# Kernel tuning notes

Hardware: AMD Instinct MI355X
Metric: run time of the kernel (lower is better)

## Reference

```python
import jax, jax.numpy as jnp
import numpy as np

N_NODES = 50000
N_EDGES = 800000
N_GRAPHS = 64
D_IN = 128
DIMS = (256, 256)


def _glorot(key, shape):
    fan_in, fan_out = shape[0], shape[1]
    lim = jnp.sqrt(6.0 / (fan_in + fan_out)).astype(jnp.float32)
    return jax.random.uniform(key, shape, jnp.float32, -lim, lim)


def setup_inputs() -> dict:
    key = jax.random.key(0)
    ks = jax.random.split(key, 12)
    x = jax.random.normal(ks[0], (N_NODES, D_IN), dtype=jnp.float32)
    edge_index = jax.random.randint(ks[1], (2, N_EDGES), 0, N_NODES, dtype=jnp.int64)
    batch = jnp.sort(jax.random.randint(ks[2], (N_NODES,), 0, N_GRAPHS, dtype=jnp.int64))
    # MLP params per GIN layer: Linear(in,dim) -> ReLU -> Linear(dim,dim) -> ReLU
    W1_0 = _glorot(ks[3], (D_IN, DIMS[0]))
    b1_0 = jnp.zeros((DIMS[0],), jnp.float32)
    W2_0 = _glorot(ks[4], (DIMS[0], DIMS[0]))
    b2_0 = jnp.zeros((DIMS[0],), jnp.float32)
    W1_1 = _glorot(ks[5], (DIMS[0], DIMS[1]))
    b1_1 = jnp.zeros((DIMS[1],), jnp.float32)
    W2_1 = _glorot(ks[6], (DIMS[1], DIMS[1]))
    b2_1 = jnp.zeros((DIMS[1],), jnp.float32)
    return {"x": x, "edge_index": edge_index, "batch": batch,
            "W1_0": W1_0, "b1_0": b1_0, "W2_0": W2_0, "b2_0": b2_0,
            "W1_1": W1_1, "b1_1": b1_1, "W2_1": W2_1, "b2_1": b2_1}


def _gin_layer(x, src, dst, W1, b1, W2, b2):
    # aggregate: sum of neighbor features (messages from src into dst)
    agg = jax.ops.segment_sum(x[src], dst, num_segments=N_NODES)
    h = x + agg  # (1 + eps) * x + agg, eps = 0
    h = jax.nn.relu(h @ W1 + b1)
    h = jax.nn.relu(h @ W2 + b2)
    return h


def reference(x, edge_index, batch, W1_0, b1_0, W2_0, b2_0, W1_1, b1_1, W2_1, b2_1):
    src, dst = edge_index[0], edge_index[1]
    h = _gin_layer(x, src, dst, W1_0, b1_0, W2_0, b2_0)
    h = _gin_layer(h, src, dst, W1_1, b1_1, W2_1, b2_1)
    # global mean pool over graphs
    sums = jax.ops.segment_sum(h, batch, num_segments=N_GRAPHS)
    counts = jax.ops.segment_sum(jnp.ones((h.shape[0],), h.dtype), batch, num_segments=N_GRAPHS)
    return sums / jnp.maximum(counts, 1.0)[:, None]
```

## Files before the change

kernel.cpp:

```cpp
#include <hip/hip_runtime.h>


typedef __bf16 bf16x8 __attribute__((ext_vector_type(8)));
typedef float f32x4 __attribute__((ext_vector_type(4)));

#define N_NODES 50000
#define N_EDGES 800000
#define N_GRAPHS 64
#define SCAN_BLOCKS 196

#define PB_HIST0 3125
#define PB_P0    6250
#define PB_P1    6378
#define PB_P2    6634
#define PB_P3    6890
#define PB_BIAS  7146
#define PB_TOTAL 7150

#define OFF_FLAGS  0ull
#define OFF_WB     64ull
#define OFF_WP0    4096ull
#define OFF_WP1    (OFF_WP0 + 65536ull)
#define OFF_WP2    (OFF_WP1 + 131072ull)
#define OFF_WP3    (OFF_WP2 + 131072ull)
#define OFF_CNT    462848ull
#define OFF_ROWPTR 662864ull
#define OFF_CURSOR 862880ull
#define OFF_SSRC   1062912ull
#define OFF_A      2662912ull
#define OFF_B      15462912ull
#define OFF_C      41062912ull
#define OFF_POOL32 66662912ull
#define OFF_BSUM   66728448ull
#define OFF_DCNT   66730496ull
#define OFF_DCUR   66731520ull
#define OFF_PERM   66732544ull

__device__ __forceinline__ float b2f(unsigned short u) {
  union { unsigned int i; float f; } v; v.i = ((unsigned int)u) << 16; return v.f;
}
__device__ __forceinline__ float b2f_lo(unsigned int u) {
  union { unsigned int i; float f; } v; v.i = u << 16; return v.f;
}
__device__ __forceinline__ float b2f_hi(unsigned int u) {
  union { unsigned int i; float f; } v; v.i = u & 0xffff0000u; return v.f;
}
__device__ __forceinline__ unsigned short f2b(float f) {
  union { unsigned int i; float f; } v; v.f = f;
  unsigned int r = v.i + 0x7fffu + ((v.i >> 16) & 1u);
  return (unsigned short)(r >> 16);
}

__global__ void detect_zero(const unsigned int* __restrict__ xw,
                            const unsigned int* __restrict__ eiw,
                            int* __restrict__ flags,
                            int* __restrict__ counts, float* __restrict__ pool32,
                            int* __restrict__ dcnt) {
  if (blockIdx.x == 0) {
    __shared__ int s_f[256], s_i[256];
    int t = threadIdx.x;
    int fh = 0, iz = 0;
    for (int i = t; i < 1024; i += 256) {
      unsigned int e = (xw[i] >> 7) & 0xFFu;
      fh += (e >= 115u && e <= 130u) ? 1 : 0;
      iz += (eiw[2 * i + 1] == 0u) ? 1 : 0;
    }
    s_f[t] = fh; s_i[t] = iz;
    __syncthreads();
    for (int s = 128; s > 0; s >>= 1) {
      if (t < s) { s_f[t] += s_f[t + s]; s_i[t] += s_i[t + s]; }
      __syncthreads();
    }
    if (t == 0) { flags[0] = s_f[0] > 512 ? 1 : 0; flags[1] = s_i[0] > 512 ? 1 : 0; }
  } else {
    int i = (blockIdx.x - 1) * 256 + threadIdx.x;
    if (i < N_NODES) counts[i] = 0;
    if (i < N_GRAPHS * 256) pool32[i] = 0.f;
    if (i < 256) dcnt[i] = 0;
  }
}

__device__ __forceinline__ void pack_w_elem(const void* W, unsigned short* Wp,
                                            int e, int isb) {
  int n = e & 255;
  int krow = e >> 8;
  int kb = krow >> 5, r = krow & 31;
  int q = r >> 3, j = r & 7;
  size_t out = ((((size_t)(kb << 8) + n) << 2) + q) * 8 + j;
  Wp[out] = isb ? ((const unsigned short*)W)[e] : f2b(((const float*)W)[e]);
}

__global__ void prep_kernel(const void* __restrict__ x, const int* __restrict__ ei,
                            const void* W0, const void* W1, const void* W2, const void* W3,
                            const void* b0, const void* b1, const void* b2, const void* b3,
                            unsigned short* __restrict__ A,
                            int* __restrict__ counts,
                            unsigned short* __restrict__ Wp0, unsigned short* __restrict__ Wp1,
                            unsigned short* __restrict__ Wp2, unsigned short* __restrict__ Wp3,
                            unsigned short* __restrict__ Wb,
                            const int* __restrict__ flags) {
  int b = blockIdx.x, t = threadIdx.x;
  int isb = flags[0];
  if (b < PB_HIST0) {
    if (!isb) {
      int i = b * 256 + t;
      const float4* f = (const float4*)x;
      float4 a = f[2 * i], c = f[2 * i + 1];
      ushort4 o0; o0.x = f2b(a.x); o0.y = f2b(a.y); o0.z = f2b(a.z); o0.w = f2b(a.w);
      ushort4 o1; o1.x = f2b(c.x); o1.y = f2b(c.y); o1.z = f2b(c.z); o1.w = f2b(c.w);
      ((ushort4*)A)[2 * i] = o0;
      ((ushort4*)A)[2 * i + 1] = o1;
    }
  } else if (b < PB_P0) {
    int e = (b - PB_HIST0) * 256 + t;
    int dst = flags[1] ? ei[2 * (N_EDGES + e)] : ei[N_EDGES + e];
    atomicAdd(&counts[dst], 1);
  } else if (b < PB_P1) {
    pack_w_elem(W0, Wp0, (b - PB_P0) * 256 + t, isb);
  } else if (b < PB_P2) {
    pack_w_elem(W1, Wp1, (b - PB_P1) * 256 + t, isb);
  } else if (b < PB_P3) {
    pack_w_elem(W2, Wp2, (b - PB_P2) * 256 + t, isb);
  } else if (b < PB_BIAS) {
    pack_w_elem(W3, Wp3, (b - PB_P3) * 256 + t, isb);
  } else {
    int i = (b - PB_BIAS) * 256 + t;
    const void* p = (i < 256) ? b0 : (i < 512) ? b1 : (i < 768) ? b2 : b3;
    int n = i & 255;
    Wb[i] = isb ? ((const unsigned short*)p)[n] : f2b(((const float*)p)[n]);
  }
}

__global__ void scan_blocks(const int* __restrict__ counts,
                            int* __restrict__ rowptr, int* __restrict__ bsum,
                            int* __restrict__ dcnt) {
  __shared__ int sd[256], lh[256];
  int t = threadIdx.x;
  int i = blockIdx.x * 256 + t;
  int v = (i < N_NODES) ? counts[i] : 0;
  sd[t] = v;
  lh[t] = 0;
  __syncthreads();
  if (i < N_NODES) atomicAdd(&lh[v > 255 ? 255 : v], 1);
  __syncthreads();
  if (lh[t] > 0) atomicAdd(&dcnt[t], lh[t]);
  for (int off = 1; off < 256; off <<= 1) {
    int u = (t >= off) ? sd[t - off] : 0;
    __syncthreads();
    sd[t] += u;
    __syncthreads();
  }
  if (i < N_NODES) rowptr[i] = sd[t] - v;
  if (t == 255) bsum[blockIdx.x] = sd[255];
}

__global__ void deg_scan(const int* __restrict__ dcnt, int* __restrict__ dcur) {
  __shared__ int sd[256];
  int t = threadIdx.x;
  int v = dcnt[t];
  sd[t] = v;
  __syncthreads();
  for (int off = 1; off < 256; off <<= 1) {
    int u = (t >= off) ? sd[t - off] : 0;
    __syncthreads();
    sd[t] += u;
    __syncthreads();
  }
  dcur[t] = sd[t] - v;
}

__global__ void scan_fix(int* __restrict__ rowptr, int* __restrict__ cursor,
                         const int* __restrict__ bsum, const int* __restrict__ counts,
                         int* __restrict__ dcur, int* __restrict__ perm) {
  __shared__ int sb[256], base[256], lc[256];
  int t = threadIdx.x;
  sb[t] = (t < SCAN_BLOCKS) ? bsum[t] : 0;
  lc[t] = 0;
  __syncthreads();
  for (int off = 1; off < 256; off <<= 1) {
    int u = (t >= off) ? sb[t - off] : 0;
    __syncthreads();
    sb[t] += u;
    __syncthreads();
  }
  int boffv = (blockIdx.x > 0) ? sb[blockIdx.x - 1] : 0;
  int i = blockIdx.x * 256 + t;
  int d = 0;
  if (i < N_NODES) {
    int v = rowptr[i] + boffv;
    rowptr[i] = v;
    cursor[i] = v;
    int c = counts[i];
    d = c > 255 ? 255 : c;
    atomicAdd(&lc[d], 1);
  }
  if (i == 0) rowptr[N_NODES] = N_EDGES;
  __syncthreads();
  int cnt = lc[t];
  base[t] = (cnt > 0) ? atomicAdd(&dcur[t], cnt) : 0;
  __syncthreads();
  lc[t] = 0;
  __syncthreads();
  if (i < N_NODES) {
    int r = atomicAdd(&lc[d], 1);
    perm[base[d] + r] = i;
  }
}

__global__ void fill_kernel(const int* __restrict__ ei, int* __restrict__ cursor,
                            unsigned short* __restrict__ ssrc,
                            const int* __restrict__ flags) {
  int e = blockIdx.x * blockDim.x + threadIdx.x;
  if (e >= N_EDGES) return;
  int is64 = flags[1];
  int src = is64 ? ei[2 * e] : ei[e];
  int dst = is64 ? ei[2 * (N_EDGES + e)] : ei[N_EDGES + e];
  int pos = atomicAdd(&cursor[dst], 1);
  ssrc[pos] = (unsigned short)src;
}

__global__ void fused_gather_gemm(const unsigned short* __restrict__ featCanon,
                                  const unsigned short* __restrict__ featRaw,
                                  const int* __restrict__ rowptr,
                                  const unsigned short* __restrict__ ssrc,
                                  const int* __restrict__ perm,
                                  const unsigned short* __restrict__ Wp,
                                  const unsigned short* __restrict__ Wb, int bias_row,
                                  unsigned short* __restrict__ C, int D,
                                  const int* __restrict__ flags) {
  __shared__ __align__(16) unsigned short Alds[16 * 264];
  __shared__ int sp[16];
  const int S = D + 8;
  const int row0 = blockIdx.x << 4;
  const int lane = threadIdx.x & 63;
  const int wave = threadIdx.x >> 6;
  const unsigned short* feat = flags[0] ? featRaw : featCanon;
  if (threadIdx.x < 16) sp[threadIdx.x] = perm[row0 + threadIdx.x];
  __syncthreads();

  {
    int sub = lane >> 4;
    int l = lane & 15;
    int nl = (wave << 2) + sub;
    int node = sp[nl];
    int beg = rowptr[node], end = rowptr[node + 1];
    int c = l << 3;
    if (D == 256) {
      const unsigned short* spt = feat + (size_t)node * 256 + c;
      uint4 sv0 = *(const uint4*)spt;
      uint4 sv1 = *(const uint4*)(spt + 128);
      float a0 = b2f_lo(sv0.x), a1 = b2f_hi(sv0.x), a2 = b2f_lo(sv0.y), a3 = b2f_hi(sv0.y);
      float a4 = b2f_lo(sv0.z), a5 = b2f_hi(sv0.z), a6 = b2f_lo(sv0.w), a7 = b2f_hi(sv0.w);
      float a8 = b2f_lo(sv1.x), a9 = b2f_hi(sv1.x), aA = b2f_lo(sv1.y), aB = b2f_hi(sv1.y);
      float aC = b2f_lo(sv1.z), aD = b2f_hi(sv1.z), aE = b2f_lo(sv1.w), aF = b2f_hi(sv1.w);
      int i = beg;
      for (; i + 1 < end; i += 2) {
        int s0 = ssrc[i], s1 = ssrc[i + 1];
        const unsigned short* p0 = feat + (size_t)s0 * 256 + c;
        const unsigned short* p1 = feat + (size_t)s1 * 256 + c;
        uint4 v00 = *(const uint4*)p0;
        uint4 v01 = *(const uint4*)(p0 + 128);
        uint4 v10 = *(const uint4*)p1;
        uint4 v11 = *(const uint4*)(p1 + 128);
        a0 += b2f_lo(v00.x); a1 += b2f_hi(v00.x); a2 += b2f_lo(v00.y); a3 += b2f_hi(v00.y);
        a4 += b2f_lo(v00.z); a5 += b2f_hi(v00.z); a6 += b2f_lo(v00.w); a7 += b2f_hi(v00.w);
        a8 += b2f_lo(v01.x); a9 += b2f_hi(v01.x); aA += b2f_lo(v01.y); aB += b2f_hi(v01.y);
        aC += b2f_lo(v01.z); aD += b2f_hi(v01.z); aE += b2f_lo(v01.w); aF += b2f_hi(v01.w);
        a0 += b2f_lo(v10.x); a1 += b2f_hi(v10.x); a2 += b2f_lo(v10.y); a3 += b2f_hi(v10.y);
        a4 += b2f_lo(v10.z); a5 += b2f_hi(v10.z); a6 += b2f_lo(v10.w); a7 += b2f_hi(v10.w);
        a8 += b2f_lo(v11.x); a9 += b2f_hi(v11.x); aA += b2f_lo(v11.y); aB += b2f_hi(v11.y);
        aC += b2f_lo(v11.z); aD += b2f_hi(v11.z); aE += b2f_lo(v11.w); aF += b2f_hi(v11.w);
      }
      if (i < end) {
        const unsigned short* p0 = feat + (size_t)ssrc[i] * 256 + c;
        uint4 v00 = *(const uint4*)p0;
        uint4 v01 = *(const uint4*)(p0 + 128);
        a0 += b2f_lo(v00.x); a1 += b2f_hi(v00.x); a2 += b2f_lo(v00.y); a3 += b2f_hi(v00.y);
        a4 += b2f_lo(v00.z); a5 += b2f_hi(v00.z); a6 += b2f_lo(v00.w); a7 += b2f_hi(v00.w);
        a8 += b2f_lo(v01.x); a9 += b2f_hi(v01.x); aA += b2f_lo(v01.y); aB += b2f_hi(v01.y);
        aC += b2f_lo(v01.z); aD += b2f_hi(v01.z); aE += b2f_lo(v01.w); aF += b2f_hi(v01.w);
      }
      uint4 o0, o1;
      o0.x = ((unsigned int)f2b(a1) << 16) | f2b(a0);
      o0.y = ((unsigned int)f2b(a3) << 16) | f2b(a2);
      o0.z = ((unsigned int)f2b(a5) << 16) | f2b(a4);
      o0.w = ((unsigned int)f2b(a7) << 16) | f2b(a6);
      o1.x = ((unsigned int)f2b(a9) << 16) | f2b(a8);
      o1.y = ((unsigned int)f2b(aB) << 16) | f2b(aA);
      o1.z = ((unsigned int)f2b(aD) << 16) | f2b(aC);
      o1.w = ((unsigned int)f2b(aF) << 16) | f2b(aE);
      *(uint4*)(&Alds[nl * S + c]) = o0;
      *(uint4*)(&Alds[nl * S + c + 128]) = o1;
    } else {
      const unsigned short* spt = feat + (size_t)node * 128 + c;
      uint4 sv0 = *(const uint4*)spt;
      float a0 = b2f_lo(sv0.x), a1 = b2f_hi(sv0.x), a2 = b2f_lo(sv0.y), a3 = b2f_hi(sv0.y);
      float a4 = b2f_lo(sv0.z), a5 = b2f_hi(sv0.z), a6 = b2f_lo(sv0.w), a7 = b2f_hi(sv0.w);
      int i = beg;
      for (; i + 1 < end; i += 2) {
        int s0 = ssrc[i], s1 = ssrc[i + 1];
        uint4 v0 = *(const uint4*)(feat + (size_t)s0 * 128 + c);
        uint4 v1 = *(const uint4*)(feat + (size_t)s1 * 128 + c);
        a0 += b2f_lo(v0.x); a1 += b2f_hi(v0.x); a2 += b2f_lo(v0.y); a3 += b2f_hi(v0.y);
        a4 += b2f_lo(v0.z); a5 += b2f_hi(v0.z); a6 += b2f_lo(v0.w); a7 += b2f_hi(v0.w);
        a0 += b2f_lo(v1.x); a1 += b2f_hi(v1.x); a2 += b2f_lo(v1.y); a3 += b2f_hi(v1.y);
        a4 += b2f_lo(v1.z); a5 += b2f_hi(v1.z); a6 += b2f_lo(v1.w); a7 += b2f_hi(v1.w);
      }
      if (i < end) {
        uint4 v0 = *(const uint4*)(feat + (size_t)ssrc[i] * 128 + c);
        a0 += b2f_lo(v0.x); a1 += b2f_hi(v0.x); a2 += b2f_lo(v0.y); a3 += b2f_hi(v0.y);
        a4 += b2f_lo(v0.z); a5 += b2f_hi(v0.z); a6 += b2f_lo(v0.w); a7 += b2f_hi(v0.w);
      }
      uint4 o0;
      o0.x = ((unsigned int)f2b(a1) << 16) | f2b(a0);
      o0.y = ((unsigned int)f2b(a3) << 16) | f2b(a2);
      o0.z = ((unsigned int)f2b(a5) << 16) | f2b(a4);
      o0.w = ((unsigned int)f2b(a7) << 16) | f2b(a6);
      *(uint4*)(&Alds[nl * S + c]) = o0;
    }
  }
  __syncthreads();

  const int m = lane & 15;
  const int q = lane >> 4;
  f32x4 acc[4];
#pragma unroll
  for (int t = 0; t < 4; ++t) acc[t] = (f32x4){0.f, 0.f, 0.f, 0.f};

  const unsigned short* arow = &Alds[m * S + (q << 3)];
  const int nb = (wave << 6) + m;
  const int kblocks = D >> 5;
  for (int kb = 0; kb < kblocks; ++kb) {
    bf16x8 af = *(const bf16x8*)(arow + (kb << 5));
    const unsigned short* wp = Wp + (((size_t)(kb << 8) + nb) * 4 + q) * 8;
    bf16x8 b0 = *(const bf16x8*)(wp);
    bf16x8 b1 = *(const bf16x8*)(wp + 512);
    bf16x8 b2 = *(const bf16x8*)(wp + 1024);
    bf16x8 b3 = *(const bf16x8*)(wp + 1536);
    acc[0] = __builtin_amdgcn_mfma_f32_16x16x32_bf16(af, b0, acc[0], 0, 0, 0);
    acc[1] = __builtin_amdgcn_mfma_f32_16x16x32_bf16(af, b1, acc[1], 0, 0, 0);
    acc[2] = __builtin_amdgcn_mfma_f32_16x16x32_bf16(af, b2, acc[2], 0, 0, 0);
    acc[3] = __builtin_amdgcn_mfma_f32_16x16x32_bf16(af, b3, acc[3], 0, 0, 0);
  }
#pragma unroll
  for (int t = 0; t < 4; ++t) {
    int n = (wave << 6) + (t << 4) + m;
    float bv = b2f(Wb[bias_row * 256 + n]);
#pragma unroll
    for (int i = 0; i < 4; ++i) {
      int r = sp[(q << 2) + i];
      float v = fmaxf(acc[t][i] + bv, 0.f);
      C[(size_t)r * 256 + n] = f2b(v);
    }
  }
}

__global__ void gemm_relu(const unsigned short* __restrict__ A,
                          const unsigned short* __restrict__ Wp,
                          const unsigned short* __restrict__ Wb, int bias_row,
                          unsigned short* __restrict__ C, int K) {
  const int row0 = blockIdx.x << 4;
  const int lane = threadIdx.x & 63;
  const int wave = threadIdx.x >> 6;
  const int m = lane & 15;
  const int q = lane >> 4;
  f32x4 acc[4];
#pragma unroll
  for (int t = 0; t < 4; ++t) acc[t] = (f32x4){0.f, 0.f, 0.f, 0.f};

  const unsigned short* arow = A + (size_t)(row0 + m) * K + (q << 3);
  const int nb = (wave << 6) + m;
  const int kblocks = K >> 5;
  for (int kb = 0; kb < kblocks; ++kb) {
    bf16x8 af = *(const bf16x8*)(arow + (kb << 5));
    const unsigned short* wp = Wp + (((size_t)(kb << 8) + nb) * 4 + q) * 8;
    bf16x8 b0 = *(const bf16x8*)(wp);
    bf16x8 b1 = *(const bf16x8*)(wp + 512);
    bf16x8 b2 = *(const bf16x8*)(wp + 1024);
    bf16x8 b3 = *(const bf16x8*)(wp + 1536);
    acc[0] = __builtin_amdgcn_mfma_f32_16x16x32_bf16(af, b0, acc[0], 0, 0, 0);
    acc[1] = __builtin_amdgcn_mfma_f32_16x16x32_bf16(af, b1, acc[1], 0, 0, 0);
    acc[2] = __builtin_amdgcn_mfma_f32_16x16x32_bf16(af, b2, acc[2], 0, 0, 0);
    acc[3] = __builtin_amdgcn_mfma_f32_16x16x32_bf16(af, b3, acc[3], 0, 0, 0);
  }
#pragma unroll
  for (int t = 0; t < 4; ++t) {
    int n = (wave << 6) + (t << 4) + m;
    float bv = b2f(Wb[bias_row * 256 + n]);
#pragma unroll
    for (int i = 0; i < 4; ++i) {
      int r = row0 + (q << 2) + i;
      float v = fmaxf(acc[t][i] + bv, 0.f);
      C[(size_t)r * 256 + n] = f2b(v);
    }
  }
}

__global__ void gemm_pool(const unsigned short* __restrict__ A,
                          const unsigned short* __restrict__ Wp,
                          const unsigned short* __restrict__ Wb, int bias_row,
                          float* __restrict__ pool32, const int* __restrict__ batch,
                          const int* __restrict__ flags, int K) {
  __shared__ int sg[16];
  const int row0 = blockIdx.x << 4;
  const int lane = threadIdx.x & 63;
  const int wave = threadIdx.x >> 6;
  if (threadIdx.x < 16) {
    int r = row0 + threadIdx.x;
    sg[threadIdx.x] = flags[1] ? batch[2 * r] : batch[r];
  }
  __syncthreads();

  const int m = lane & 15;
  const int q = lane >> 4;
  f32x4 acc[4];
#pragma unroll
  for (int t = 0; t < 4; ++t) acc[t] = (f32x4){0.f, 0.f, 0.f, 0.f};

  const unsigned short* arow = A + (size_t)(row0 + m) * K + (q << 3);
  const int nb = (wave << 6) + m;
  const int kblocks = K >> 5;
  for (int kb = 0; kb < kblocks; ++kb) {
    bf16x8 af = *(const bf16x8*)(arow + (kb << 5));
    const unsigned short* wp = Wp + (((size_t)(kb << 8) + nb) * 4 + q) * 8;
    bf16x8 b0 = *(const bf16x8*)(wp);
    bf16x8 b1 = *(const bf16x8*)(wp + 512);
    bf16x8 b2 = *(const bf16x8*)(wp + 1024);
    bf16x8 b3 = *(const bf16x8*)(wp + 1536);
    acc[0] = __builtin_amdgcn_mfma_f32_16x16x32_bf16(af, b0, acc[0], 0, 0, 0);
    acc[1] = __builtin_amdgcn_mfma_f32_16x16x32_bf16(af, b1, acc[1], 0, 0, 0);
    acc[2] = __builtin_amdgcn_mfma_f32_16x16x32_bf16(af, b2, acc[2], 0, 0, 0);
    acc[3] = __builtin_amdgcn_mfma_f32_16x16x32_bf16(af, b3, acc[3], 0, 0, 0);
  }

  int uniform = (sg[0] == sg[15]);
#pragma unroll
  for (int t = 0; t < 4; ++t) {
    int n = (wave << 6) + (t << 4) + m;
    float bv = b2f(Wb[bias_row * 256 + n]);
    float v0 = fmaxf(acc[t][0] + bv, 0.f);
    float v1 = fmaxf(acc[t][1] + bv, 0.f);
    float v2 = fmaxf(acc[t][2] + bv, 0.f);
    float v3 = fmaxf(acc[t][3] + bv, 0.f);
    if (uniform) {
      float ps = v0 + v1 + v2 + v3;
      ps += __shfl_xor(ps, 16);
      ps += __shfl_xor(ps, 32);
      if (q == 0) unsafeAtomicAdd(&pool32[sg[0] * 256 + n], ps);
    } else {
      int gp = sg[q << 2];
      float a = 0.f;
      float vv[4] = {v0, v1, v2, v3};
#pragma unroll
      for (int i = 0; i < 4; ++i) {
        int g = sg[(q << 2) + i];
        if (g != gp) { unsafeAtomicAdd(&pool32[gp * 256 + n], a); a = 0.f; gp = g; }
        a += vv[i];
      }
      unsafeAtomicAdd(&pool32[gp * 256 + n], a);
    }
  }
}

__device__ __forceinline__ int lower_bound(const int* a, int n, int v, int is64) {
  int lo = 0, hi = n;
  while (lo < hi) {
    int mid = (lo + hi) >> 1;
    int bv = is64 ? a[2 * mid] : a[mid];
    if (bv < v) lo = mid + 1; else hi = mid;
  }
  return lo;
}

__global__ void pool_final(const float* __restrict__ pool32,
                           const int* __restrict__ batch,
                           void* __restrict__ out,
                           const int* __restrict__ flags) {
  __shared__ int sh[2];
  int g = blockIdx.x;
  int is64 = flags[1];
  if (threadIdx.x == 0) sh[0] = lower_bound(batch, N_NODES, g, is64);
  if (threadIdx.x == 1) sh[1] = lower_bound(batch, N_NODES, g + 1, is64);
  __syncthreads();
  int c = threadIdx.x;
  float res = pool32[g * 256 + c] / fmaxf((float)(sh[1] - sh[0]), 1.0f);
  if (flags[0]) ((unsigned short*)out)[(size_t)g * 256 + c] = f2b(res);
  else          ((float*)out)[(size_t)g * 256 + c] = res;
}

extern "C" void kernel_launch(void* const* d_in, const int* in_sizes, int n_in,
                              void* d_out, int out_size, void* d_ws, size_t ws_size,
                              hipStream_t stream) {
  const void* x    = d_in[0];
  const int*  ei   = (const int*)d_in[1];
  const int*  batch= (const int*)d_in[2];

  char* ws = (char*)d_ws;
  int*            flags = (int*)(ws + OFF_FLAGS);
  unsigned short* Wb    = (unsigned short*)(ws + OFF_WB);
  unsigned short* Wp0   = (unsigned short*)(ws + OFF_WP0);
  unsigned short* Wp1   = (unsigned short*)(ws + OFF_WP1);
  unsigned short* Wp2   = (unsigned short*)(ws + OFF_WP2);
  unsigned short* Wp3   = (unsigned short*)(ws + OFF_WP3);
  int*            cnts  = (int*)(ws + OFF_CNT);
  int*            rowp  = (int*)(ws + OFF_ROWPTR);
  int*            curs  = (int*)(ws + OFF_CURSOR);
  unsigned short* ssrc  = (unsigned short*)(ws + OFF_SSRC);
  unsigned short* A     = (unsigned short*)(ws + OFF_A);
  unsigned short* B     = (unsigned short*)(ws + OFF_B);
  unsigned short* C     = (unsigned short*)(ws + OFF_C);
  float*          pool32= (float*)(ws + OFF_POOL32);
  int*            bsum  = (int*)(ws + OFF_BSUM);
  int*            dcnt  = (int*)(ws + OFF_DCNT);
  int*            dcur  = (int*)(ws + OFF_DCUR);
  int*            perm  = (int*)(ws + OFF_PERM);

  detect_zero<<<197, 256, 0, stream>>>((const unsigned int*)x, (const unsigned int*)ei,
                                       flags, cnts, pool32, dcnt);
  prep_kernel<<<PB_TOTAL, 256, 0, stream>>>(x, ei,
                                            d_in[3], d_in[5], d_in[7], d_in[9],
                                            d_in[4], d_in[6], d_in[8], d_in[10],
                                            A, cnts, Wp0, Wp1, Wp2, Wp3, Wb, flags);
  scan_blocks<<<SCAN_BLOCKS, 256, 0, stream>>>(cnts, rowp, bsum, dcnt);
  deg_scan<<<1, 256, 0, stream>>>(dcnt, dcur);
  scan_fix<<<SCAN_BLOCKS, 256, 0, stream>>>(rowp, curs, bsum, cnts, dcur, perm);
  fill_kernel<<<3125, 256, 0, stream>>>(ei, curs, ssrc, flags);

  fused_gather_gemm<<<3125, 256, 0, stream>>>(A, (const unsigned short*)x, rowp, ssrc,
                                              perm, Wp0, Wb, 0, C, 128, flags);
  gemm_relu<<<3125, 256, 0, stream>>>(C, Wp1, Wb, 1, B, 256);

  fused_gather_gemm<<<3125, 256, 0, stream>>>(B, B, rowp, ssrc,
                                              perm, Wp2, Wb, 2, C, 256, flags);
  gemm_pool<<<3125, 256, 0, stream>>>(C, Wp3, Wb, 3, pool32, batch, flags, 256);

  pool_final<<<N_GRAPHS, 256, 0, stream>>>(pool32, batch, d_out, flags);
}
```

Before: 383.7 us.

## Replicate pool accumulators, fold degree scan into scan_fix, unroll gather by four

Pooling atomics now target one of eight replicated per-graph accumulator buffers chosen by block index, and pool_final sums the replicas. This is meant to cut atomic contention on the 64x256 pool array. The single-block deg_scan kernel is removed: every scan_fix block recomputes the degree-histogram prefix locally, and dcur is now zeroed as a counter. The gather loop is unrolled to four edges per iteration so more loads are in flight, at the cost of more registers.

After: 378.2 us. About the same (-1.4%).

```diff
diff --git a/kernel.cpp b/kernel.cpp
--- a/kernel.cpp
+++ b/kernel.cpp
@@ -8,6 +8,7 @@
 #define N_EDGES 800000
 #define N_GRAPHS 64
 #define SCAN_BLOCKS 196
+#define NREP 8
 
 #define PB_HIST0 3125
 #define PB_P0    6250
@@ -31,10 +32,10 @@
 #define OFF_B      15462912ull
 #define OFF_C      41062912ull
 #define OFF_POOL32 66662912ull
-#define OFF_BSUM   66728448ull
-#define OFF_DCNT   66730496ull
-#define OFF_DCUR   66731520ull
-#define OFF_PERM   66732544ull
+#define OFF_BSUM   67187200ull
+#define OFF_DCNT   67189248ull
+#define OFF_DCUR   67190272ull
+#define OFF_PERM   67191296ull
 
 __device__ __forceinline__ float b2f(unsigned short u) {
   union { unsigned int i; float f; } v; v.i = ((unsigned int)u) << 16; return v.f;
@@ -50,12 +51,21 @@
   unsigned int r = v.i + 0x7fffu + ((v.i >> 16) & 1u);
   return (unsigned short)(r >> 16);
 }
+__device__ __forceinline__ unsigned int pk2(float hi, float lo) {
+  return ((unsigned int)f2b(hi) << 16) | f2b(lo);
+}
+__device__ __forceinline__ void acc8(float* a, uint4 v) {
+  a[0] += b2f_lo(v.x); a[1] += b2f_hi(v.x);
+  a[2] += b2f_lo(v.y); a[3] += b2f_hi(v.y);
+  a[4] += b2f_lo(v.z); a[5] += b2f_hi(v.z);
+  a[6] += b2f_lo(v.w); a[7] += b2f_hi(v.w);
+}
 
 __global__ void detect_zero(const unsigned int* __restrict__ xw,
                             const unsigned int* __restrict__ eiw,
                             int* __restrict__ flags,
                             int* __restrict__ counts, float* __restrict__ pool32,
-                            int* __restrict__ dcnt) {
+                            int* __restrict__ dcnt, int* __restrict__ dcur) {
   if (blockIdx.x == 0) {
     __shared__ int s_f[256], s_i[256];
     int t = threadIdx.x;
@@ -75,8 +85,8 @@
   } else {
     int i = (blockIdx.x - 1) * 256 + threadIdx.x;
     if (i < N_NODES) counts[i] = 0;
-    if (i < N_GRAPHS * 256) pool32[i] = 0.f;
-    if (i < 256) dcnt[i] = 0;
+    if (i < NREP * N_GRAPHS * 256) pool32[i] = 0.f;
+    if (i < 256) { dcnt[i] = 0; dcur[i] = 0; }
   }
 }
 
@@ -154,35 +164,25 @@
   if (t == 255) bsum[blockIdx.x] = sd[255];
 }
 
-__global__ void deg_scan(const int* __restrict__ dcnt, int* __restrict__ dcur) {
-  __shared__ int sd[256];
-  int t = threadIdx.x;
-  int v = dcnt[t];
-  sd[t] = v;
-  __syncthreads();
-  for (int off = 1; off < 256; off <<= 1) {
-    int u = (t >= off) ? sd[t - off] : 0;
-    __syncthreads();
-    sd[t] += u;
-    __syncthreads();
-  }
-  dcur[t] = sd[t] - v;
-}
-
 __global__ void scan_fix(int* __restrict__ rowptr, int* __restrict__ cursor,
                          const int* __restrict__ bsum, const int* __restrict__ counts,
-                         int* __restrict__ dcur, int* __restrict__ perm) {
-  __shared__ int sb[256], base[256], lc[256];
+                         const int* __restrict__ dcnt, int* __restrict__ dcur,
+                         int* __restrict__ perm) {
+  __shared__ int sb[256], db[256], base[256], lc[256];
   int t = threadIdx.x;
   sb[t] = (t < SCAN_BLOCKS) ? bsum[t] : 0;
+  db[t] = dcnt[t];
   lc[t] = 0;
   __syncthreads();
   for (int off = 1; off < 256; off <<= 1) {
-    int u = (t >= off) ? sb[t - off] : 0;
+    int u1 = (t >= off) ? sb[t - off] : 0;
+    int u2 = (t >= off) ? db[t - off] : 0;
     __syncthreads();
-    sb[t] += u;
+    sb[t] += u1; db[t] += u2;
     __syncthreads();
   }
+  db[t] -= dcnt[t];
+  __syncthreads();
   int boffv = (blockIdx.x > 0) ? sb[blockIdx.x - 1] : 0;
   int i = blockIdx.x * 256 + t;
   int d = 0;
@@ -197,7 +197,7 @@
   if (i == 0) rowptr[N_NODES] = N_EDGES;
   __syncthreads();
   int cnt = lc[t];
-  base[t] = (cnt > 0) ? atomicAdd(&dcur[t], cnt) : 0;
+  base[t] = (cnt > 0) ? (db[t] + atomicAdd(&dcur[t], cnt)) : 0;
   __syncthreads();
   lc[t] = 0;
   __syncthreads();
@@ -246,76 +246,61 @@
     int beg = rowptr[node], end = rowptr[node + 1];
     int c = l << 3;
     if (D == 256) {
+      float a[16];
+#pragma unroll
+      for (int j = 0; j < 16; ++j) a[j] = 0.f;
       const unsigned short* spt = feat + (size_t)node * 256 + c;
-      uint4 sv0 = *(const uint4*)spt;
-      uint4 sv1 = *(const uint4*)(spt + 128);
-      float a0 = b2f_lo(sv0.x), a1 = b2f_hi(sv0.x), a2 = b2f_lo(sv0.y), a3 = b2f_hi(sv0.y);
-      float a4 = b2f_lo(sv0.z), a5 = b2f_hi(sv0.z), a6 = b2f_lo(sv0.w), a7 = b2f_hi(sv0.w);
-      float a8 = b2f_lo(sv1.x), a9 = b2f_hi(sv1.x), aA = b2f_lo(sv1.y), aB = b2f_hi(sv1.y);
-      float aC = b2f_lo(sv1.z), aD = b2f_hi(sv1.z), aE = b2f_lo(sv1.w), aF = b2f_hi(sv1.w);
+      acc8(a, *(const uint4*)spt);
+      acc8(a + 8, *(const uint4*)(spt + 128));
       int i = beg;
-      for (; i + 1 < end; i += 2) {
-        int s0 = ssrc[i], s1 = ssrc[i + 1];
-        const unsigned short* p0 = feat + (size_t)s0 * 256 + c;
-        const unsigned short* p1 = feat + (size_t)s1 * 256 + c;
-        uint4 v00 = *(const uint4*)p0;
-        uint4 v01 = *(const uint4*)(p0 + 128);
-        uint4 v10 = *(const uint4*)p1;
-        uint4 v11 = *(const uint4*)(p1 + 128);
-        a0 += b2f_lo(v00.x); a1 += b2f_hi(v00.x); a2 += b2f_lo(v00.y); a3 += b2f_hi(v00.y);
-        a4 += b2f_lo(v00.z); a5 += b2f_hi(v00.z); a6 += b2f_lo(v00.w); a7 += b2f_hi(v00.w);
-        a8 += b2f_lo(v01.x); a9 += b2f_hi(v01.x); aA += b2f_lo(v01.y); aB += b2f_hi(v01.y);
-        aC += b2f_lo(v01.z); aD += b2f_hi(v01.z); aE += b2f_lo(v01.w); aF += b2f_hi(v01.w);
-        a0 += b2f_lo(v10.x); a1 += b2f_hi(v10.x); a2 += b2f_lo(v10.y); a3 += b2f_hi(v10.y);
-        a4 += b2f_lo(v10.z); a5 += b2f_hi(v10.z); a6 += b2f_lo(v10.w); a7 += b2f_hi(v10.w);
-        a8 += b2f_lo(v11.x); a9 += b2f_hi(v11.x); aA += b2f_lo(v11.y); aB += b2f_hi(v11.y);
-        aC += b2f_lo(v11.z); aD += b2f_hi(v11.z); aE += b2f_lo(v11.w); aF += b2f_hi(v11.w);
+      for (; i + 3 < end; i += 4) {
+        int ss[4];
+#pragma unroll
+        for (int e = 0; e < 4; ++e) ss[e] = ssrc[i + e];
+        uint4 v[8];
+#pragma unroll
+        for (int e = 0; e < 4; ++e) {
+          const unsigned short* p = feat + (size_t)ss[e] * 256 + c;
+          v[2 * e] = *(const uint4*)p;
+          v[2 * e + 1] = *(const uint4*)(p + 128);
+        }
+#pragma unroll
+        for (int e = 0; e < 4; ++e) { acc8(a, v[2 * e]); acc8(a + 8, v[2 * e + 1]); }
       }
-      if (i < end) {
-        const unsigned short* p0 = feat + (size_t)ssrc[i] * 256 + c;
-        uint4 v00 = *(const uint4*)p0;
-        uint4 v01 = *(const uint4*)(p0 + 128);
-        a0 += b2f_lo(v00.x); a1 += b2f_hi(v00.x); a2 += b2f_lo(v00.y); a3 += b2f_hi(v00.y);
-        a4 += b2f_lo(v00.z); a5 += b2f_hi(v00.z); a6 += b2f_lo(v00.w); a7 += b2f_hi(v00.w);
-        a8 += b2f_lo(v01.x); a9 += b2f_hi(v01.x); aA += b2f_lo(v01.y); aB += b2f_hi(v01.y);
-        aC += b2f_lo(v01.z); aD += b2f_hi(v01.z); aE += b2f_lo(v01.w); aF += b2f_hi(v01.w);
+      for (; i < end; ++i) {
+        const unsigned short* p = feat + (size_t)ssrc[i] * 256 + c;
+        acc8(a, *(const uint4*)p);
+        acc8(a + 8, *(const uint4*)(p + 128));
       }
       uint4 o0, o1;
-      o0.x = ((unsigned int)f2b(a1) << 16) | f2b(a0);
-      o0.y = ((unsigned int)f2b(a3) << 16) | f2b(a2);
-      o0.z = ((unsigned int)f2b(a5) << 16) | f2b(a4);
-      o0.w = ((unsigned int)f2b(a7) << 16) | f2b(a6);
-      o1.x = ((unsigned int)f2b(a9) << 16) | f2b(a8);
-      o1.y = ((unsigned int)f2b(aB) << 16) | f2b(aA);
-      o1.z = ((unsigned int)f2b(aD) << 16) | f2b(aC);
-      o1.w = ((unsigned int)f2b(aF) << 16) | f2b(aE);
+      o0.x = pk2(a[1], a[0]);  o0.y = pk2(a[3], a[2]);
+      o0.z = pk2(a[5], a[4]);  o0.w = pk2(a[7], a[6]);
+      o1.x = pk2(a[9], a[8]);  o1.y = pk2(a[11], a[10]);
+      o1.z = pk2(a[13], a[12]); o1.w = pk2(a[15], a[14]);
       *(uint4*)(&Alds[nl * S + c]) = o0;
       *(uint4*)(&Alds[nl * S + c + 128]) = o1;
     } else {
-      const unsigned short* spt = feat + (size_t)node * 128 + c;
-      uint4 sv0 = *(const uint4*)spt;
-      float a0 = b2f_lo(sv0.x), a1 = b2f_hi(sv0.x), a2 = b2f_lo(sv0.y), a3 = b2f_hi(sv0.y);
-      float a4 = b2f_lo(sv0.z), a5 = b2f_hi(sv0.z), a6 = b2f_lo(sv0.w), a7 = b2f_hi(sv0.w);
+      float a[8];
+#pragma unroll
+      for (int j = 0; j < 8; ++j) a[j] = 0.f;
+      acc8(a, *(const uint4*)(feat + (size_t)node * 128 + c));
       int i = beg;
-      for (; i + 1 < end; i += 2) {
-        int s0 = ssrc[i], s1 = ssrc[i + 1];
-        uint4 v0 = *(const uint4*)(feat + (size_t)s0 * 128 + c);
-        uint4 v1 = *(const uint4*)(feat + (size_t)s1 * 128 + c);
-        a0 += b2f_lo(v0.x); a1 += b2f_hi(v0.x); a2 += b2f_lo(v0.y); a3 += b2f_hi(v0.y);
-        a4 += b2f_lo(v0.z); a5 += b2f_hi(v0.z); a6 += b2f_lo(v0.w); a7 += b2f_hi(v0.w);
-        a0 += b2f_lo(v1.x); a1 += b2f_hi(v1.x); a2 += b2f_lo(v1.y); a3 += b2f_hi(v1.y);
-        a4 += b2f_lo(v1.z); a5 += b2f_hi(v1.z); a6 += b2f_lo(v1.w); a7 += b2f_hi(v1.w);
+      for (; i + 3 < end; i += 4) {
+        int ss[4];
+#pragma unroll
+        for (int e = 0; e < 4; ++e) ss[e] = ssrc[i + e];
+        uint4 v[4];
+#pragma unroll
+        for (int e = 0; e < 4; ++e)
+          v[e] = *(const uint4*)(feat + (size_t)ss[e] * 128 + c);
+#pragma unroll
+        for (int e = 0; e < 4; ++e) acc8(a, v[e]);
       }
-      if (i < end) {
-        uint4 v0 = *(const uint4*)(feat + (size_t)ssrc[i] * 128 + c);
-        a0 += b2f_lo(v0.x); a1 += b2f_hi(v0.x); a2 += b2f_lo(v0.y); a3 += b2f_hi(v0.y);
-        a4 += b2f_lo(v0.z); a5 += b2f_hi(v0.z); a6 += b2f_lo(v0.w); a7 += b2f_hi(v0.w);
-      }
+      for (; i < end; ++i)
+        acc8(a, *(const uint4*)(feat + (size_t)ssrc[i] * 128 + c));
       uint4 o0;
-      o0.x = ((unsigned int)f2b(a1) << 16) | f2b(a0);
-      o0.y = ((unsigned int)f2b(a3) << 16) | f2b(a2);
-      o0.z = ((unsigned int)f2b(a5) << 16) | f2b(a4);
-      o0.w = ((unsigned int)f2b(a7) << 16) | f2b(a6);
+      o0.x = pk2(a[1], a[0]); o0.y = pk2(a[3], a[2]);
+      o0.z = pk2(a[5], a[4]); o0.w = pk2(a[7], a[6]);
       *(uint4*)(&Alds[nl * S + c]) = o0;
     }
   }
@@ -405,6 +390,7 @@
   const int row0 = blockIdx.x << 4;
   const int lane = threadIdx.x & 63;
   const int wave = threadIdx.x >> 6;
+  float* pr = pool32 + ((blockIdx.x & (NREP - 1)) << 14);
   if (threadIdx.x < 16) {
     int r = row0 + threadIdx.x;
     sg[threadIdx.x] = flags[1] ? batch[2 * r] : batch[r];
@@ -446,7 +432,7 @@
       float ps = v0 + v1 + v2 + v3;
       ps += __shfl_xor(ps, 16);
       ps += __shfl_xor(ps, 32);
-      if (q == 0) unsafeAtomicAdd(&pool32[sg[0] * 256 + n], ps);
+      if (q == 0) unsafeAtomicAdd(&pr[sg[0] * 256 + n], ps);
     } else {
       int gp = sg[q << 2];
       float a = 0.f;
@@ -454,10 +440,10 @@
 #pragma unroll
       for (int i = 0; i < 4; ++i) {
         int g = sg[(q << 2) + i];
-        if (g != gp) { unsafeAtomicAdd(&pool32[gp * 256 + n], a); a = 0.f; gp = g; }
+        if (g != gp) { unsafeAtomicAdd(&pr[gp * 256 + n], a); a = 0.f; gp = g; }
         a += vv[i];
       }
-      unsafeAtomicAdd(&pool32[gp * 256 + n], a);
+      unsafeAtomicAdd(&pr[gp * 256 + n], a);
     }
   }
 }
@@ -483,7 +469,10 @@
   if (threadIdx.x == 1) sh[1] = lower_bound(batch, N_NODES, g + 1, is64);
   __syncthreads();
   int c = threadIdx.x;
-  float res = pool32[g * 256 + c] / fmaxf((float)(sh[1] - sh[0]), 1.0f);
+  float s = 0.f;
+#pragma unroll
+  for (int r = 0; r < NREP; ++r) s += pool32[(r << 14) + g * 256 + c];
+  float res = s / fmaxf((float)(sh[1] - sh[0]), 1.0f);
   if (flags[0]) ((unsigned short*)out)[(size_t)g * 256 + c] = f2b(res);
   else          ((float*)out)[(size_t)g * 256 + c] = res;
 }
@@ -515,15 +504,14 @@
   int*            dcur  = (int*)(ws + OFF_DCUR);
   int*            perm  = (int*)(ws + OFF_PERM);
 
-  detect_zero<<<197, 256, 0, stream>>>((const unsigned int*)x, (const unsigned int*)ei,
-                                       flags, cnts, pool32, dcnt);
+  detect_zero<<<513, 256, 0, stream>>>((const unsigned int*)x, (const unsigned int*)ei,
+                                       flags, cnts, pool32, dcnt, dcur);
   prep_kernel<<<PB_TOTAL, 256, 0, stream>>>(x, ei,
                                             d_in[3], d_in[5], d_in[7], d_in[9],
                                             d_in[4], d_in[6], d_in[8], d_in[10],
                                             A, cnts, Wp0, Wp1, Wp2, Wp3, Wb, flags);
   scan_blocks<<<SCAN_BLOCKS, 256, 0, stream>>>(cnts, rowp, bsum, dcnt);
-  deg_scan<<<1, 256, 0, stream>>>(dcnt, dcur);
-  scan_fix<<<SCAN_BLOCKS, 256, 0, stream>>>(rowp, curs, bsum, cnts, dcur, perm);
+  scan_fix<<<SCAN_BLOCKS, 256, 0, stream>>>(rowp, curs, bsum, cnts, dcnt, dcur, perm);
   fill_kernel<<<3125, 256, 0, stream>>>(ei, curs, ssrc, flags);
 
   fused_gather_gemm<<<3125, 256, 0, stream>>>(A, (const unsigned short*)x, rowp, ssrc,
```
